# Kernel optimization log

Measured on AMD Instinct MI355X. Metric: run time of the kernel, lower is better.

## Reference

```python
import jax, jax.numpy as jnp
import numpy as np

V, E, H, S, B = 50000, 512, 1024, 512, 64
N_TAGS = 13
D_FF = 256
N_OUT = 1


def setup_inputs() -> dict:
    key = jax.random.key(0)
    ks = jax.random.split(key, 12)
    s_e = 1.0 / np.sqrt(H)  # torch LSTMCell init scale
    return {
        "tokens": jax.random.randint(ks[0], (B, S), 0, V),
        "tags": jax.random.randint(ks[1], (S,), 0, N_TAGS),
        "emb_w": jax.random.normal(ks[2], (V, E), jnp.float32),
        "W_ih": jax.random.uniform(ks[3], (N_TAGS, 4 * H, E), jnp.float32, -s_e, s_e),
        "W_hh": jax.random.uniform(ks[4], (N_TAGS, 4 * H, H), jnp.float32, -s_e, s_e),
        "b_ih": jax.random.uniform(ks[5], (N_TAGS, 4 * H), jnp.float32, -s_e, s_e),
        "b_hh": jax.random.uniform(ks[6], (N_TAGS, 4 * H), jnp.float32, -s_e, s_e),
        "W1": jax.random.normal(ks[7], (D_FF, H), jnp.float32) * 0.02,
        "b1": jnp.zeros((D_FF,), jnp.float32),
        "W2": jax.random.normal(ks[8], (N_OUT, D_FF), jnp.float32) * 0.02,
        "b2": jnp.zeros((N_OUT,), jnp.float32),
    }


def _lstm_scan(x_seq, tags, W_ih, W_hh, b_ih, b_hh):
    # x_seq: [S, B, E]; per-step weights selected by tag index (tag-routed LSTMCell).
    Bsz = x_seq.shape[1]
    Hs = W_hh.shape[-1]

    def step(carry, inp):
        h, c = carry
        x_t, tag = inp
        wi, wh = W_ih[tag], W_hh[tag]          # [4H,E], [4H,H]
        bias = b_ih[tag] + b_hh[tag]            # [4H]
        gates = x_t @ wi.T + h @ wh.T + bias    # [B,4H]
        i, f, g, o = jnp.split(gates, 4, axis=-1)  # torch order: i,f,g,o
        c = jax.nn.sigmoid(f) * c + jax.nn.sigmoid(i) * jnp.tanh(g)
        h = jax.nn.sigmoid(o) * jnp.tanh(c)
        return (h, c), None

    h0 = jnp.zeros((Bsz, Hs), x_seq.dtype)
    (h, c), _ = jax.lax.scan(step, (h0, h0), (x_seq, tags))
    return h


def reference(tokens, tags, emb_w, W_ih, W_hh, b_ih, b_hh, W1, b1, W2, b2):
    x = emb_w[tokens]                 # [B,S,E] embedding lookup
    x_seq = jnp.swapaxes(x, 0, 1)     # [S,B,E]
    h = _lstm_scan(x_seq, tags, W_ih, W_hh, b_ih, b_hh)  # final hidden [B,H]
    hidden = jax.nn.relu(h @ W1.T + b1)  # dropout is identity at eval
    out = hidden @ W2.T + b2             # [B,1]
    out = jax.nn.sigmoid(out)            # non-multiclass branch
    return jnp.squeeze(out, axis=1)      # [B]
```

## Files before the change

### kernel.cpp

```cpp
#include <hip/hip_runtime.h>
#include <hip/hip_bf16.h>
#include <hip/hip_cooperative_groups.h>

namespace cg = cooperative_groups;

typedef __attribute__((ext_vector_type(8))) short short8;
typedef __attribute__((ext_vector_type(4))) float f32x4;
typedef unsigned long long ull;

static constexpr int E_ = 512, H_ = 1024, S_ = 512, B_ = 64, NT_ = 13;
static constexpr int G4H = 4 * H_;

static constexpr size_t WIH_ELEMS = (size_t)NT_ * G4H * E_;
static constexpr size_t WHH_ELEMS = (size_t)NT_ * G4H * H_;
static constexpr size_t X_ELEMS   = (size_t)S_ * B_ * E_;
static constexpr size_t BIAS_ELEMS = (size_t)NT_ * G4H;
static constexpr size_t HBUF_ELEMS = (size_t)B_ * H_;

static constexpr size_t OFF_WIH  = 0;
static constexpr size_t OFF_WHH  = OFF_WIH + WIH_ELEMS * 2;
static constexpr size_t OFF_X    = OFF_WHH + WHH_ELEMS * 2;
static constexpr size_t OFF_BIAS = OFF_X + X_ELEMS * 2;
static constexpr size_t OFF_H    = OFF_BIAS + BIAS_ELEMS * 4;
static constexpr size_t OFF_FLAGS = OFF_H + 2 * HBUF_ELEMS * 2;

static constexpr int BH_STRIDE = 1032;

__device__ inline short f2bf(float x) {
  __hip_bfloat16 h = __float2bfloat16(x);
  return __builtin_bit_cast(short, h);
}
__device__ inline float b2f(short s) {
  unsigned u = ((unsigned)(unsigned short)s) << 16;
  return __builtin_bit_cast(float, u);
}
__device__ inline short8 cvt8(const float* src) {
  f32x4 a = *(const f32x4*)src;
  f32x4 b = *(const f32x4*)(src + 4);
  short8 o;
  o[0] = f2bf(a[0]); o[1] = f2bf(a[1]); o[2] = f2bf(a[2]); o[3] = f2bf(a[3]);
  o[4] = f2bf(b[0]); o[5] = f2bf(b[1]); o[6] = f2bf(b[2]); o[7] = f2bf(b[3]);
  return o;
}
__device__ inline float sigm(float x) { return 1.f / (1.f + __expf(-x)); }

__device__ inline int unpack_row(int p) {
  return ((p >> 2) & 3) * H_ + (p >> 4) * 4 + (p & 3);
}

__device__ inline void stage16(const short* g, short* l) {
  __builtin_amdgcn_global_load_lds(
      (const __attribute__((address_space(1))) void*)g,
      (__attribute__((address_space(3))) void*)l, 16, 0, 0);
}

__device__ inline f32x4 xgemm(const short* __restrict__ x_bf,
                              const short* __restrict__ wih_pk,
                              int t, int tag, int wg, int m0, int arow, int kq) {
  const short* ap = x_bf + ((size_t)t * B_ + m0 + arow) * E_ + kq;
  const short* bp = wih_pk + ((size_t)tag * G4H + wg * 16 + arow) * E_ + kq;
  short8 av[16], bv[16];
#pragma unroll
  for (int i = 0; i < 16; ++i) av[i] = *(const short8*)(ap + i * 32);
#pragma unroll
  for (int i = 0; i < 16; ++i) bv[i] = *(const short8*)(bp + i * 32);
  f32x4 a = {0.f, 0.f, 0.f, 0.f};
#pragma unroll
  for (int i = 0; i < 16; ++i)
    a = __builtin_amdgcn_mfma_f32_16x16x32_bf16(av[i], bv[i], a, 0, 0, 0);
  return a;
}

__global__ __launch_bounds__(256, 1) void lstm_tag_kernel(
    const int* __restrict__ tokens, const int* __restrict__ tags,
    const float* __restrict__ emb_w,
    const float* __restrict__ W_ih, const float* __restrict__ W_hh,
    const float* __restrict__ b_ih, const float* __restrict__ b_hh,
    const float* __restrict__ W1, const float* __restrict__ b1,
    const float* __restrict__ W2, const float* __restrict__ b2,
    float* __restrict__ out,
    short* __restrict__ wih_pk, short* __restrict__ whh_pk,
    short* __restrict__ x_bf, float* __restrict__ bias_pk,
    short* __restrict__ h_bf, unsigned* __restrict__ flags) {
  cg::grid_group grid = cg::this_grid();
  const int tid = threadIdx.x;
  const int wg = blockIdx.x;
  const int lane = tid & 63;
  const int ll = tid >> 6;
  const int gw = wg * 4 + ll;
  const int gtid = wg * 256 + tid;

  __shared__ short lds_bh[16 * BH_STRIDE];
  __shared__ float lds_tile[4 * 256];
  __shared__ ull lds_hst_q[32];
  short* lds_hst = (short*)lds_hst_q;

  for (int row = gw; row < NT_ * G4H; row += 1024) {
    int tag = row >> 12, p = row & 4095, r = unpack_row(p);
    const float* src = W_ih + ((size_t)tag * G4H + r) * E_ + lane * 8;
    short* dst = wih_pk + ((size_t)tag * G4H + p) * E_ + lane * 8;
    *(short8*)dst = cvt8(src);
  }
  for (int row = gw; row < NT_ * G4H; row += 1024) {
    int tag = row >> 12, p = row & 4095, r = unpack_row(p);
    const float* src = W_hh + ((size_t)tag * G4H + r) * H_;
    short* dst = whh_pk + ((size_t)tag * G4H + p) * H_;
    *(short8*)(dst + lane * 8) = cvt8(src + lane * 8);
    *(short8*)(dst + 512 + lane * 8) = cvt8(src + 512 + lane * 8);
  }
  for (int idx = gtid; idx < NT_ * G4H; idx += 65536) {
    int tag = idx >> 12;
    int r = unpack_row(idx & 4095);
    bias_pk[idx] = b_ih[tag * G4H + r] + b_hh[tag * G4H + r];
  }
  for (int row = gw; row < S_ * B_; row += 1024) {
    int t = row >> 6, b = row & 63;
    int tok = tokens[b * S_ + t];
    const float* src = emb_w + (size_t)tok * E_ + lane * 8;
    short* dst = x_bf + (size_t)row * E_ + lane * 8;
    *(short8*)dst = cvt8(src);
  }
  ((int*)h_bf)[gtid] = 0;
  if (gtid < 256) flags[gtid] = 0u;

  grid.sync();

  const int arow = lane & 15;
  const int kq = (lane >> 4) * 8;
  const int m0 = ll * 16;

  int tag = tags[0];
  {
    const short* src = whh_pk + ((size_t)tag * G4H + wg * 16) * H_;
#pragma unroll
    for (int rr = 0; rr < 4; ++rr) {
      int r = ll * 4 + rr;
      const short* g = src + r * H_ + lane * 8;
      stage16(g, &lds_bh[r * BH_STRIDE]);
      stage16(g + 512, &lds_bh[r * BH_STRIDE + 512]);
    }
  }
  f32x4 acc_x = xgemm(x_bf, wih_pk, 0, tag, wg, m0, arow, kq);
  asm volatile("s_waitcnt vmcnt(0)" ::: "memory");
  __syncthreads();

  float c_reg = 0.f;

  for (int t = 0; t < S_; ++t) {
    const short* Acur = h_bf + (size_t)(t & 1) * HBUF_ELEMS;
    short* Anext = h_bf + (size_t)((t + 1) & 1) * HBUF_ELEMS;

    ull* ab = (ull*)(Acur + (size_t)(m0 + arow) * H_);
    const int ib = kq >> 2;
    short8 ah[32];
#pragma unroll
    for (int i = 0; i < 32; ++i) {
      ull lo = __hip_atomic_load(ab + ib + i * 8, __ATOMIC_RELAXED,
                                 __HIP_MEMORY_SCOPE_AGENT);
      ull hi = __hip_atomic_load(ab + ib + i * 8 + 1, __ATOMIC_RELAXED,
                                 __HIP_MEMORY_SCOPE_AGENT);
      union { ull q[2]; short8 s; } u;
      u.q[0] = lo; u.q[1] = hi;
      ah[i] = u.s;
    }

    const short* bph = &lds_bh[arow * BH_STRIDE + kq];
    f32x4 acc0 = acc_x;
    f32x4 acc1 = {0.f, 0.f, 0.f, 0.f};
#pragma unroll
    for (int i = 0; i < 16; ++i) {
      short8 b0 = *(const short8*)(bph + (2 * i) * 32);
      short8 b1v = *(const short8*)(bph + (2 * i + 1) * 32);
      acc0 = __builtin_amdgcn_mfma_f32_16x16x32_bf16(ah[2 * i], b0, acc0, 0, 0, 0);
      acc1 = __builtin_amdgcn_mfma_f32_16x16x32_bf16(ah[2 * i + 1], b1v, acc1, 0, 0, 0);
    }
    const float biasv = bias_pk[tag * G4H + wg * 16 + arow];

    float* tl = lds_tile + ll * 256;
#pragma unroll
    for (int r = 0; r < 4; ++r)
      tl[((lane >> 4) * 4 + r) * 16 + arow] = acc0[r] + acc1[r] + biasv;
    __builtin_amdgcn_wave_barrier();
    {
      const int u = lane & 3, brow = lane >> 2;
      const float* rp = tl + brow * 16;
      float iv = rp[u], fv = rp[4 + u], gv = rp[8 + u], ov = rp[12 + u];
      float cn = sigm(fv) * c_reg + sigm(iv) * tanhf(gv);
      c_reg = cn;
      float hn = sigm(ov) * tanhf(cn);
      lds_hst[(m0 + brow) * 4 + u] = f2bf(hn);
    }

    __syncthreads();

    if (ll == 0) {
      ull v = *(const ull*)&lds_hst[lane * 4];
      __hip_atomic_store((ull*)(Anext + (size_t)lane * H_ + wg * 4), v,
                         __ATOMIC_RELAXED, __HIP_MEMORY_SCOPE_AGENT);
      asm volatile("s_waitcnt vmcnt(0)" ::: "memory");
      if (lane == 0)
        __hip_atomic_store(flags + wg, (unsigned)(t + 1), __ATOMIC_RELAXED,
                           __HIP_MEMORY_SCOPE_AGENT);
    }

    if (t < S_ - 1) {
      const int tagn = tags[t + 1];
      acc_x = xgemm(x_bf, wih_pk, t + 1, tagn, wg, m0, arow, kq);
      const short* src = whh_pk + ((size_t)tagn * G4H + wg * 16) * H_;
#pragma unroll
      for (int rr = 0; rr < 4; ++rr) {
        int r = ll * 4 + rr;
        const short* g = src + r * H_ + lane * 8;
        stage16(g, &lds_bh[r * BH_STRIDE]);
        stage16(g + 512, &lds_bh[r * BH_STRIDE + 512]);
      }
      tag = tagn;
    }
    asm volatile("s_waitcnt vmcnt(0)" ::: "memory");

    if (ll == 0) {
      const unsigned target = (unsigned)(t + 1);
      for (;;) {
        unsigned v0 = __hip_atomic_load(flags + lane, __ATOMIC_RELAXED,
                                        __HIP_MEMORY_SCOPE_AGENT);
        unsigned v1 = __hip_atomic_load(flags + lane + 64, __ATOMIC_RELAXED,
                                        __HIP_MEMORY_SCOPE_AGENT);
        unsigned v2 = __hip_atomic_load(flags + lane + 128, __ATOMIC_RELAXED,
                                        __HIP_MEMORY_SCOPE_AGENT);
        unsigned v3 = __hip_atomic_load(flags + lane + 192, __ATOMIC_RELAXED,
                                        __HIP_MEMORY_SCOPE_AGENT);
        unsigned m01 = v0 < v1 ? v0 : v1;
        unsigned m23 = v2 < v3 ? v2 : v3;
        unsigned mn = m01 < m23 ? m01 : m23;
        if (__all((int)(mn >= target))) break;
        __builtin_amdgcn_s_sleep(1);
      }
    }
    __syncthreads();
  }

  grid.sync();

  if (wg < B_) {
    const int b = wg, d = tid;
    const short* hrow = h_bf + (size_t)(S_ & 1) * HBUF_ELEMS + (size_t)b * H_;
    const float* w1r = W1 + (size_t)d * H_;
    float s = b1[d];
#pragma unroll 4
    for (int k = 0; k < H_; k += 8) {
      short8 hv = *(const short8*)(hrow + k);
      f32x4 w0 = *(const f32x4*)(w1r + k);
      f32x4 w1v = *(const f32x4*)(w1r + k + 4);
      s += w0[0] * b2f(hv[0]) + w0[1] * b2f(hv[1]) + w0[2] * b2f(hv[2]) +
           w0[3] * b2f(hv[3]) + w1v[0] * b2f(hv[4]) + w1v[1] * b2f(hv[5]) +
           w1v[2] * b2f(hv[6]) + w1v[3] * b2f(hv[7]);
    }
    s = fmaxf(s, 0.f);
    __shared__ float red[256];
    red[tid] = s * W2[d];
    __syncthreads();
    for (int off = 128; off > 0; off >>= 1) {
      if (tid < off) red[tid] += red[tid + off];
      __syncthreads();
    }
    if (tid == 0) out[b] = 1.f / (1.f + __expf(-(red[0] + b2[0])));
  }
}

extern "C" void kernel_launch(void* const* d_in, const int* in_sizes, int n_in,
                              void* d_out, int out_size, void* d_ws, size_t ws_size,
                              hipStream_t stream) {
  const int* tokens = (const int*)d_in[0];
  const int* tags = (const int*)d_in[1];
  const float* emb_w = (const float*)d_in[2];
  const float* W_ih = (const float*)d_in[3];
  const float* W_hh = (const float*)d_in[4];
  const float* b_ih = (const float*)d_in[5];
  const float* b_hh = (const float*)d_in[6];
  const float* W1 = (const float*)d_in[7];
  const float* b1 = (const float*)d_in[8];
  const float* W2 = (const float*)d_in[9];
  const float* b2 = (const float*)d_in[10];
  float* out = (float*)d_out;

  char* ws = (char*)d_ws;
  short* wih_pk = (short*)(ws + OFF_WIH);
  short* whh_pk = (short*)(ws + OFF_WHH);
  short* x_bf = (short*)(ws + OFF_X);
  float* bias_pk = (float*)(ws + OFF_BIAS);
  short* h_bf = (short*)(ws + OFF_H);
  unsigned* flags = (unsigned*)(ws + OFF_FLAGS);

  void* args[] = {&tokens, &tags, &emb_w, &W_ih, &W_hh, &b_ih, &b_hh,
                  &W1, &b1, &W2, &b2, &out,
                  &wih_pk, &whh_pk, &x_bf, &bias_pk, &h_bf, &flags};
  dim3 grid(256), block(256);
  hipLaunchCooperativeKernel(reinterpret_cast<void*>(&lstm_tag_kernel), grid,
                             block, args, 0, stream);
}
```

Measured before the change: 6.829 ms.

## Run recurrence on 64 workgroups with per-wave flags and global W_hh reads

The recurrent loop now runs on 64 workgroups, each owning 64 gate rows, instead of all 256 workgroups owning 16 rows each. Every wave runs four MFMA chains over 16 columns each, publishes its own h slice and flag, and polls the flags independently, so the per-step __syncthreads is gone. W_hh is read straight from global memory (L2) each step rather than staged into LDS, and the spare workgroups only sleep until the flag shows the final step. Fewer participants should make the grid barrier cheaper, at the cost of four times more MFMA and weight traffic per workgroup on the critical path.

```diff
diff --git a/kernel.cpp b/kernel.cpp
--- a/kernel.cpp
+++ b/kernel.cpp
@@ -10,6 +10,8 @@
 
 static constexpr int E_ = 512, H_ = 1024, S_ = 512, B_ = 64, NT_ = 13;
 static constexpr int G4H = 4 * H_;
+static constexpr int NWG = 64;
+static constexpr int RPW = 64;
 
 static constexpr size_t WIH_ELEMS = (size_t)NT_ * G4H * E_;
 static constexpr size_t WHH_ELEMS = (size_t)NT_ * G4H * H_;
@@ -24,7 +26,7 @@
 static constexpr size_t OFF_H    = OFF_BIAS + BIAS_ELEMS * 4;
 static constexpr size_t OFF_FLAGS = OFF_H + 2 * HBUF_ELEMS * 2;
 
-static constexpr int BH_STRIDE = 1032;
+static constexpr int TL_STRIDE = 68;
 
 __device__ inline short f2bf(float x) {
   __hip_bfloat16 h = __float2bfloat16(x);
@@ -48,27 +50,28 @@
   return ((p >> 2) & 3) * H_ + (p >> 4) * 4 + (p & 3);
 }
 
-__device__ inline void stage16(const short* g, short* l) {
-  __builtin_amdgcn_global_load_lds(
-      (const __attribute__((address_space(1))) void*)g,
-      (__attribute__((address_space(3))) void*)l, 16, 0, 0);
-}
-
-__device__ inline f32x4 xgemm(const short* __restrict__ x_bf,
+__device__ inline void xgemm4(const short* __restrict__ x_bf,
                               const short* __restrict__ wih_pk,
-                              int t, int tag, int wg, int m0, int arow, int kq) {
+                              int t, int tag, int wg, int m0, int arow, int kq,
+                              f32x4& o0, f32x4& o1, f32x4& o2, f32x4& o3) {
   const short* ap = x_bf + ((size_t)t * B_ + m0 + arow) * E_ + kq;
-  const short* bp = wih_pk + ((size_t)tag * G4H + wg * 16 + arow) * E_ + kq;
-  short8 av[16], bv[16];
+  short8 av[16];
 #pragma unroll
   for (int i = 0; i < 16; ++i) av[i] = *(const short8*)(ap + i * 32);
-#pragma unroll
-  for (int i = 0; i < 16; ++i) bv[i] = *(const short8*)(bp + i * 32);
-  f32x4 a = {0.f, 0.f, 0.f, 0.f};
-#pragma unroll
-  for (int i = 0; i < 16; ++i)
-    a = __builtin_amdgcn_mfma_f32_16x16x32_bf16(av[i], bv[i], a, 0, 0, 0);
-  return a;
+  const short* b0p = wih_pk + ((size_t)tag * G4H + wg * RPW + arow) * E_ + kq;
+  const short* b1p = b0p + (size_t)16 * E_;
+  const short* b2p = b0p + (size_t)32 * E_;
+  const short* b3p = b0p + (size_t)48 * E_;
+  f32x4 a0 = {0.f, 0.f, 0.f, 0.f}, a1 = {0.f, 0.f, 0.f, 0.f};
+  f32x4 a2 = {0.f, 0.f, 0.f, 0.f}, a3 = {0.f, 0.f, 0.f, 0.f};
+#pragma unroll
+  for (int i = 0; i < 16; ++i) {
+    a0 = __builtin_amdgcn_mfma_f32_16x16x32_bf16(av[i], *(const short8*)(b0p + i * 32), a0, 0, 0, 0);
+    a1 = __builtin_amdgcn_mfma_f32_16x16x32_bf16(av[i], *(const short8*)(b1p + i * 32), a1, 0, 0, 0);
+    a2 = __builtin_amdgcn_mfma_f32_16x16x32_bf16(av[i], *(const short8*)(b2p + i * 32), a2, 0, 0, 0);
+    a3 = __builtin_amdgcn_mfma_f32_16x16x32_bf16(av[i], *(const short8*)(b3p + i * 32), a3, 0, 0, 0);
+  }
+  o0 = a0; o1 = a1; o2 = a2; o3 = a3;
 }
 
 __global__ __launch_bounds__(256, 1) void lstm_tag_kernel(
@@ -90,9 +93,8 @@
   const int gw = wg * 4 + ll;
   const int gtid = wg * 256 + tid;
 
-  __shared__ short lds_bh[16 * BH_STRIDE];
-  __shared__ float lds_tile[4 * 256];
-  __shared__ ull lds_hst_q[32];
+  __shared__ float lds_tile[4 * 16 * TL_STRIDE];
+  __shared__ ull lds_hst_q[256];
   short* lds_hst = (short*)lds_hst_q;
 
   for (int row = gw; row < NT_ * G4H; row += 1024) {
@@ -125,116 +127,125 @@
 
   grid.sync();
 
-  const int arow = lane & 15;
-  const int kq = (lane >> 4) * 8;
-  const int m0 = ll * 16;
-
-  int tag = tags[0];
-  {
-    const short* src = whh_pk + ((size_t)tag * G4H + wg * 16) * H_;
-#pragma unroll
-    for (int rr = 0; rr < 4; ++rr) {
-      int r = ll * 4 + rr;
-      const short* g = src + r * H_ + lane * 8;
-      stage16(g, &lds_bh[r * BH_STRIDE]);
-      stage16(g + 512, &lds_bh[r * BH_STRIDE + 512]);
-    }
-  }
-  f32x4 acc_x = xgemm(x_bf, wih_pk, 0, tag, wg, m0, arow, kq);
-  asm volatile("s_waitcnt vmcnt(0)" ::: "memory");
-  __syncthreads();
-
-  float c_reg = 0.f;
-
-  for (int t = 0; t < S_; ++t) {
-    const short* Acur = h_bf + (size_t)(t & 1) * HBUF_ELEMS;
-    short* Anext = h_bf + (size_t)((t + 1) & 1) * HBUF_ELEMS;
-
-    ull* ab = (ull*)(Acur + (size_t)(m0 + arow) * H_);
-    const int ib = kq >> 2;
-    short8 ah[32];
-#pragma unroll
-    for (int i = 0; i < 32; ++i) {
-      ull lo = __hip_atomic_load(ab + ib + i * 8, __ATOMIC_RELAXED,
-                                 __HIP_MEMORY_SCOPE_AGENT);
-      ull hi = __hip_atomic_load(ab + ib + i * 8 + 1, __ATOMIC_RELAXED,
-                                 __HIP_MEMORY_SCOPE_AGENT);
-      union { ull q[2]; short8 s; } u;
-      u.q[0] = lo; u.q[1] = hi;
-      ah[i] = u.s;
-    }
-
-    const short* bph = &lds_bh[arow * BH_STRIDE + kq];
-    f32x4 acc0 = acc_x;
-    f32x4 acc1 = {0.f, 0.f, 0.f, 0.f};
-#pragma unroll
-    for (int i = 0; i < 16; ++i) {
-      short8 b0 = *(const short8*)(bph + (2 * i) * 32);
-      short8 b1v = *(const short8*)(bph + (2 * i + 1) * 32);
-      acc0 = __builtin_amdgcn_mfma_f32_16x16x32_bf16(ah[2 * i], b0, acc0, 0, 0, 0);
-      acc1 = __builtin_amdgcn_mfma_f32_16x16x32_bf16(ah[2 * i + 1], b1v, acc1, 0, 0, 0);
-    }
-    const float biasv = bias_pk[tag * G4H + wg * 16 + arow];
-
-    float* tl = lds_tile + ll * 256;
-#pragma unroll
-    for (int r = 0; r < 4; ++r)
-      tl[((lane >> 4) * 4 + r) * 16 + arow] = acc0[r] + acc1[r] + biasv;
-    __builtin_amdgcn_wave_barrier();
+  if (wg < NWG) {
+    const int arow = lane & 15;
+    const int kq = (lane >> 4) * 8;
+    const int m0 = ll * 16;
+
+    int tag = tags[0];
+    f32x4 ax0, ax1, ax2, ax3;
+    xgemm4(x_bf, wih_pk, 0, tag, wg, m0, arow, kq, ax0, ax1, ax2, ax3);
+    float bs0, bs1, bs2, bs3;
     {
-      const int u = lane & 3, brow = lane >> 2;
-      const float* rp = tl + brow * 16;
-      float iv = rp[u], fv = rp[4 + u], gv = rp[8 + u], ov = rp[12 + u];
-      float cn = sigm(fv) * c_reg + sigm(iv) * tanhf(gv);
-      c_reg = cn;
-      float hn = sigm(ov) * tanhf(cn);
-      lds_hst[(m0 + brow) * 4 + u] = f2bf(hn);
-    }
-
-    __syncthreads();
-
-    if (ll == 0) {
-      ull v = *(const ull*)&lds_hst[lane * 4];
-      __hip_atomic_store((ull*)(Anext + (size_t)lane * H_ + wg * 4), v,
-                         __ATOMIC_RELAXED, __HIP_MEMORY_SCOPE_AGENT);
-      asm volatile("s_waitcnt vmcnt(0)" ::: "memory");
-      if (lane == 0)
-        __hip_atomic_store(flags + wg, (unsigned)(t + 1), __ATOMIC_RELAXED,
-                           __HIP_MEMORY_SCOPE_AGENT);
-    }
-
-    if (t < S_ - 1) {
-      const int tagn = tags[t + 1];
-      acc_x = xgemm(x_bf, wih_pk, t + 1, tagn, wg, m0, arow, kq);
-      const short* src = whh_pk + ((size_t)tagn * G4H + wg * 16) * H_;
-#pragma unroll
-      for (int rr = 0; rr < 4; ++rr) {
-        int r = ll * 4 + rr;
-        const short* g = src + r * H_ + lane * 8;
-        stage16(g, &lds_bh[r * BH_STRIDE]);
-        stage16(g + 512, &lds_bh[r * BH_STRIDE + 512]);
-      }
-      tag = tagn;
-    }
-    asm volatile("s_waitcnt vmcnt(0)" ::: "memory");
-
-    if (ll == 0) {
-      const unsigned target = (unsigned)(t + 1);
-      for (;;) {
-        unsigned v0 = __hip_atomic_load(flags + lane, __ATOMIC_RELAXED,
-                                        __HIP_MEMORY_SCOPE_AGENT);
-        unsigned v1 = __hip_atomic_load(flags + lane + 64, __ATOMIC_RELAXED,
-                                        __HIP_MEMORY_SCOPE_AGENT);
-        unsigned v2 = __hip_atomic_load(flags + lane + 128, __ATOMIC_RELAXED,
-                                        __HIP_MEMORY_SCOPE_AGENT);
-        unsigned v3 = __hip_atomic_load(flags + lane + 192, __ATOMIC_RELAXED,
-                                        __HIP_MEMORY_SCOPE_AGENT);
-        unsigned m01 = v0 < v1 ? v0 : v1;
-        unsigned m23 = v2 < v3 ? v2 : v3;
-        unsigned mn = m01 < m23 ? m01 : m23;
-        if (__all((int)(mn >= target))) break;
-        __builtin_amdgcn_s_sleep(1);
-      }
+      const float* bp_ = bias_pk + tag * G4H + wg * RPW + arow;
+      bs0 = bp_[0]; bs1 = bp_[16]; bs2 = bp_[32]; bs3 = bp_[48];
+    }
+
+    float c0 = 0.f, c1 = 0.f, c2 = 0.f, c3 = 0.f;
+
+    for (int t = 0; t < S_; ++t) {
+      const short* Acur = h_bf + (size_t)(t & 1) * HBUF_ELEMS;
+      short* Anext = h_bf + (size_t)((t + 1) & 1) * HBUF_ELEMS;
+
+      ull* ab = (ull*)(Acur + (size_t)(m0 + arow) * H_);
+      const int ib = kq >> 2;
+      short8 ah[32];
+#pragma unroll
+      for (int i = 0; i < 32; ++i) {
+        ull lo = __hip_atomic_load(ab + ib + i * 8, __ATOMIC_RELAXED,
+                                   __HIP_MEMORY_SCOPE_AGENT);
+        ull hi = __hip_atomic_load(ab + ib + i * 8 + 1, __ATOMIC_RELAXED,
+                                   __HIP_MEMORY_SCOPE_AGENT);
+        union { ull q[2]; short8 s; } u;
+        u.q[0] = lo; u.q[1] = hi;
+        ah[i] = u.s;
+      }
+
+      f32x4 a0 = ax0, a1 = ax1, a2 = ax2, a3 = ax3;
+      const short* b0p = whh_pk + ((size_t)tag * G4H + wg * RPW + arow) * H_ + kq;
+      const short* b1p = b0p + (size_t)16 * H_;
+      const short* b2p = b0p + (size_t)32 * H_;
+      const short* b3p = b0p + (size_t)48 * H_;
+#pragma unroll
+      for (int i = 0; i < 32; ++i) {
+        a0 = __builtin_amdgcn_mfma_f32_16x16x32_bf16(ah[i], *(const short8*)(b0p + i * 32), a0, 0, 0, 0);
+        a1 = __builtin_amdgcn_mfma_f32_16x16x32_bf16(ah[i], *(const short8*)(b1p + i * 32), a1, 0, 0, 0);
+        a2 = __builtin_amdgcn_mfma_f32_16x16x32_bf16(ah[i], *(const short8*)(b2p + i * 32), a2, 0, 0, 0);
+        a3 = __builtin_amdgcn_mfma_f32_16x16x32_bf16(ah[i], *(const short8*)(b3p + i * 32), a3, 0, 0, 0);
+      }
+
+      float* tlw = lds_tile + ll * (16 * TL_STRIDE);
+#pragma unroll
+      for (int r = 0; r < 4; ++r) {
+        int br = ((lane >> 4) * 4 + r) * TL_STRIDE;
+        tlw[br + 0 * 16 + arow] = a0[r] + bs0;
+        tlw[br + 1 * 16 + arow] = a1[r] + bs1;
+        tlw[br + 2 * 16 + arow] = a2[r] + bs2;
+        tlw[br + 3 * 16 + arow] = a3[r] + bs3;
+      }
+      __builtin_amdgcn_wave_barrier();
+      {
+        const int uu = lane & 3, b = lane >> 2;
+        const float* rp = tlw + b * TL_STRIDE;
+        float iv, fv, gv, ov, cn;
+        iv = rp[0 + uu]; fv = rp[4 + uu]; gv = rp[8 + uu]; ov = rp[12 + uu];
+        cn = sigm(fv) * c0 + sigm(iv) * tanhf(gv); c0 = cn;
+        lds_hst[(m0 + b) * 16 + 0 + uu] = f2bf(sigm(ov) * tanhf(cn));
+        iv = rp[16 + uu]; fv = rp[20 + uu]; gv = rp[24 + uu]; ov = rp[28 + uu];
+        cn = sigm(fv) * c1 + sigm(iv) * tanhf(gv); c1 = cn;
+        lds_hst[(m0 + b) * 16 + 4 + uu] = f2bf(sigm(ov) * tanhf(cn));
+        iv = rp[32 + uu]; fv = rp[36 + uu]; gv = rp[40 + uu]; ov = rp[44 + uu];
+        cn = sigm(fv) * c2 + sigm(iv) * tanhf(gv); c2 = cn;
+        lds_hst[(m0 + b) * 16 + 8 + uu] = f2bf(sigm(ov) * tanhf(cn));
+        iv = rp[48 + uu]; fv = rp[52 + uu]; gv = rp[56 + uu]; ov = rp[60 + uu];
+        cn = sigm(fv) * c3 + sigm(iv) * tanhf(gv); c3 = cn;
+        lds_hst[(m0 + b) * 16 + 12 + uu] = f2bf(sigm(ov) * tanhf(cn));
+      }
+      __builtin_amdgcn_wave_barrier();
+
+      {
+        const int row = m0 + (lane >> 2);
+        ull v = lds_hst_q[row * 4 + (lane & 3)];
+        __hip_atomic_store((ull*)(Anext + (size_t)row * H_ + wg * 16 + (lane & 3) * 4),
+                           v, __ATOMIC_RELAXED, __HIP_MEMORY_SCOPE_AGENT);
+        asm volatile("s_waitcnt vmcnt(0)" ::: "memory");
+        if (lane == 0)
+          __hip_atomic_store(flags + gw, (unsigned)(t + 1), __ATOMIC_RELAXED,
+                             __HIP_MEMORY_SCOPE_AGENT);
+      }
+
+      if (t < S_ - 1) {
+        const int tagn = tags[t + 1];
+        xgemm4(x_bf, wih_pk, t + 1, tagn, wg, m0, arow, kq, ax0, ax1, ax2, ax3);
+        const float* bp_ = bias_pk + tagn * G4H + wg * RPW + arow;
+        bs0 = bp_[0]; bs1 = bp_[16]; bs2 = bp_[32]; bs3 = bp_[48];
+        tag = tagn;
+      }
+
+      {
+        const unsigned target = (unsigned)(t + 1);
+        for (;;) {
+          unsigned v0 = __hip_atomic_load(flags + lane, __ATOMIC_RELAXED,
+                                          __HIP_MEMORY_SCOPE_AGENT);
+          unsigned v1 = __hip_atomic_load(flags + lane + 64, __ATOMIC_RELAXED,
+                                          __HIP_MEMORY_SCOPE_AGENT);
+          unsigned v2 = __hip_atomic_load(flags + lane + 128, __ATOMIC_RELAXED,
+                                          __HIP_MEMORY_SCOPE_AGENT);
+          unsigned v3 = __hip_atomic_load(flags + lane + 192, __ATOMIC_RELAXED,
+                                          __HIP_MEMORY_SCOPE_AGENT);
+          unsigned m01 = v0 < v1 ? v0 : v1;
+          unsigned m23 = v2 < v3 ? v2 : v3;
+          unsigned mn = m01 < m23 ? m01 : m23;
+          if (__all((int)(mn >= target))) break;
+          __builtin_amdgcn_s_sleep(1);
+        }
+      }
+    }
+  } else {
+    if (tid == 0) {
+      while (__hip_atomic_load(flags, __ATOMIC_RELAXED,
+                               __HIP_MEMORY_SCOPE_AGENT) < (unsigned)S_)
+        __builtin_amdgcn_s_sleep(127);
     }
     __syncthreads();
   }
```

New measurement: 17.31 ms. 2.53x slower.
